# Performance work log

Hardware: AMD Instinct MI355X
Metric: run time of the kernel (lower is better)

Reference implementation:

```python
import jax, jax.numpy as jnp
import numpy as np

H = 4          # num_heads
DK = 128       # head_k_dim = hidden*expand_k/H = 1024*0.5/4
DV = 256       # head_v_dim = hidden*expand_v/H
LOW_RANK = 16  # gate_low_rank_dim
GATE_NORM = 16.0  # gate_logit_normalizer
CHUNK = 64
EPS = 1e-5


def setup_inputs() -> dict:
    key = jax.random.key(0)
    ks = jax.random.split(key, 10)
    Dm = 1024
    Kd, Vd = H * DK, H * DV  # key_dim=512, value_dim=1024
    def lin(k, fan_in, fan_out):
        return jax.random.normal(k, (fan_in, fan_out), jnp.float32) * (fan_in ** -0.5)
    return {
        "x": jax.random.normal(ks[0], (4, 2048, Dm), jnp.float32),
        "Wq": lin(ks[1], Dm, Kd),
        "Wk": lin(ks[2], Dm, Kd),
        "Wv": lin(ks[3], Dm, Vd),
        "Wg": lin(ks[4], Dm, Vd),            # output gate proj
        "Wgk1": lin(ks[5], Dm, LOW_RANK),     # low-rank gate proj (no bias)
        "Wgk2": lin(ks[6], LOW_RANK, Kd),     # second gate proj (with bias)
        "bgk2": jnp.zeros((Kd,), jnp.float32),
        "Wo": lin(ks[7], Vd, Dm),
        "gnw": jnp.ones((DV,), jnp.float32),  # FusedRMSNormGated weight
    }


def _gla_chunk(q, k, v, gk):
    """Exact chunkwise evaluation of the GLA recurrence:
       S_t = diag(exp(gk_t)) S_{t-1} + k_t^T v_t;  o_t = scale * q_t S_t.
       q,k,gk: [B,T,H,DK], v: [B,T,H,DV]."""
    B, T, _, _ = q.shape
    NC, C = T // CHUNK, CHUNK
    scale = DK ** -0.5
    def chunks(a):  # [B,T,H,D] -> [NC,B,H,C,D]
        return a.reshape(B, NC, C, H, a.shape[-1]).transpose(1, 0, 3, 2, 4)
    qc, kc, vc, gc = chunks(q), chunks(k), chunks(v), chunks(gk)
    G = jnp.cumsum(gc, axis=-2)                    # within-chunk cumulative log-decay
    qg = qc * jnp.exp(G) * scale                   # q_i exp(G_i)
    k_intra = kc * jnp.exp(-G)                     # k_j exp(-G_j)
    kg = kc * jnp.exp(G[..., -1:, :] - G)          # k_j exp(G_C - G_j) for state update
    g_last = jnp.exp(G[..., -1, :])                # exp(G_C): per-chunk total decay
    # intra-chunk causal attention (diagonal included)
    A = jnp.einsum('nbhik,nbhjk->nbhij', qg, k_intra)
    A = jnp.where(jnp.tril(jnp.ones((C, C), bool)), A, 0.0)
    o_intra = jnp.einsum('nbhij,nbhjv->nbhiv', A, vc)
    def step(S, inp):
        qg_, kg_, v_, gl_, oi_ = inp
        o = oi_ + jnp.einsum('bhck,bhkv->bhcv', qg_, S)
        S = S * gl_[..., :, None] + jnp.einsum('bhck,bhcv->bhkv', kg_, v_)
        return S, o
    S0 = jnp.zeros((B, H, DK, DV), q.dtype)
    _, o = jax.lax.scan(step, S0, (qg, kg, vc, g_last, o_intra))
    return o.transpose(1, 0, 3, 2, 4).reshape(B, T, H, DV)


def reference(x, Wq, Wk, Wv, Wg, Wgk1, Wgk2, bgk2, Wo, gnw):
    B, T, Dm = x.shape
    q = (x @ Wq).reshape(B, T, H, DK)
    k = (x @ Wk).reshape(B, T, H, DK)
    v = (x @ Wv).reshape(B, T, H, DV)
    gk = jax.nn.log_sigmoid((x @ Wgk1) @ Wgk2 + bgk2) / GATE_NORM
    gk = gk.reshape(B, T, H, DK)
    o = _gla_chunk(q, k, v, gk)                              # [B,T,H,DV]
    g = (x @ Wg).reshape(B, T, H, DV)
    # FusedRMSNormGated: RMSNorm(o) * weight * swish(g)
    o = o * jax.lax.rsqrt(jnp.mean(o * o, axis=-1, keepdims=True) + EPS) * gnw
    o = o * (g * jax.nn.sigmoid(g))
    return o.reshape(B, T, H * DV) @ Wo
```

## Files before the change

kernel.cpp:

```cpp
#include <hip/hip_runtime.h>
#include <hip/hip_bf16.h>
#include <stdint.h>

#define B_  4
#define T_  2048
#define DM  1024
#define H_  4
#define DK_ 128
#define DV_ 256
#define KD  512
#define VD  1024
#define NCH 32
#define CC  64
#define BT  8192
#define SCALE 0.08838834764831845f
#define GNORM_INV 0.0625f

typedef __attribute__((ext_vector_type(8))) short short8;
typedef __attribute__((ext_vector_type(4))) float f32x4;
typedef uint32_t u32;
typedef unsigned short ushort_t;

__device__ inline ushort_t f2b(float f) {
    u32 u = __builtin_bit_cast(u32, f);
    u32 r = (u + 0x7fffu + ((u >> 16) & 1u)) >> 16;
    return (ushort_t)r;
}
__device__ inline void unpack2(u32 u, float& lo, float& hi) {
    lo = __builtin_bit_cast(float, u << 16);
    hi = __builtin_bit_cast(float, u & 0xffff0000u);
}

__global__ __launch_bounds__(256)
void cvtx(const float* __restrict__ x, ushort_t* __restrict__ xb, int n) {
    int idx = (blockIdx.x * 256 + threadIdx.x) * 8;
    if (idx >= n) return;
    float4 a = *(const float4*)&x[idx];
    float4 b = *(const float4*)&x[idx + 4];
    uint4 p;
    p.x = (u32)f2b(a.x) | ((u32)f2b(a.y) << 16);
    p.y = (u32)f2b(a.z) | ((u32)f2b(a.w) << 16);
    p.z = (u32)f2b(b.x) | ((u32)f2b(b.y) << 16);
    p.w = (u32)f2b(b.z) | ((u32)f2b(b.w) << 16);
    *(uint4*)&xb[idx] = p;
}

__global__ __launch_bounds__(256)
void tcvt(const float* __restrict__ W, ushort_t* __restrict__ Wt, int K, int N) {
    __shared__ float tile[32][33];
    const int k0 = blockIdx.x * 32, n0 = blockIdx.y * 32;
    const int r = threadIdx.x >> 3, c4 = (threadIdx.x & 7) * 4;
    float4 wv = *(const float4*)&W[(size_t)(k0 + r) * N + n0 + c4];
    tile[r][c4 + 0] = wv.x; tile[r][c4 + 1] = wv.y;
    tile[r][c4 + 2] = wv.z; tile[r][c4 + 3] = wv.w;
    __syncthreads();
    u32 lo = (u32)f2b(tile[c4 + 0][r]) | ((u32)f2b(tile[c4 + 1][r]) << 16);
    u32 hi = (u32)f2b(tile[c4 + 2][r]) | ((u32)f2b(tile[c4 + 3][r]) << 16);
    uint2 o2; o2.x = lo; o2.y = hi;
    *(uint2*)&Wt[(size_t)(n0 + r) * K + k0 + c4] = o2;
}

template<int OUTBF>
__global__ __launch_bounds__(256)
void gemm_bf16(const ushort_t* __restrict__ A, const ushort_t* __restrict__ Bt,
               void* __restrict__ Cout, int M, int N, int K) {
    __shared__ ushort_t Al[128 * 40];
    __shared__ ushort_t Bl[128 * 40];
    const int t = threadIdx.x;
    const int wave = t >> 6, lane = t & 63;
    const int wr = wave >> 1, wc = wave & 1;
    const int row0 = blockIdx.x * 128, col0 = blockIdx.y * 128;
    const int lr = t >> 2;
    const int lk8 = (t & 3) * 8;
    const int lm = lane & 15, lk = (lane >> 4) * 8;

    f32x4 acc[4][4];
    #pragma unroll
    for (int i = 0; i < 4; ++i)
        #pragma unroll
        for (int j = 0; j < 4; ++j) acc[i][j] = f32x4{0.f, 0.f, 0.f, 0.f};

    const ushort_t* Ap = A + (size_t)row0 * K;
    const ushort_t* Bp = Bt + (size_t)col0 * K;

    for (int k0 = 0; k0 < K; k0 += 32) {
        __syncthreads();
        #pragma unroll
        for (int m = 0; m < 2; ++m) {
            int r = m * 64 + lr;
            uint4 av = *(const uint4*)(Ap + (size_t)r * K + k0 + lk8);
            *(uint4*)(&Al[r * 40 + lk8]) = av;
            uint4 bv = *(const uint4*)(Bp + (size_t)r * K + k0 + lk8);
            *(uint4*)(&Bl[r * 40 + lk8]) = bv;
        }
        __syncthreads();
        short8 af[4], bfr[4];
        #pragma unroll
        for (int f = 0; f < 4; ++f)
            af[f] = *(const short8*)(&Al[(wr * 64 + f * 16 + lm) * 40 + lk]);
        #pragma unroll
        for (int f = 0; f < 4; ++f)
            bfr[f] = *(const short8*)(&Bl[(wc * 64 + f * 16 + lm) * 40 + lk]);
        #pragma unroll
        for (int i = 0; i < 4; ++i)
            #pragma unroll
            for (int j = 0; j < 4; ++j)
                acc[i][j] = __builtin_amdgcn_mfma_f32_16x16x32_bf16(af[i], bfr[j], acc[i][j], 0, 0, 0);
    }
    const int orow = row0 + wr * 64 + (lane >> 4) * 4;
    const int ocol = col0 + wc * 64 + lm;
    #pragma unroll
    for (int i = 0; i < 4; ++i)
        #pragma unroll
        for (int j = 0; j < 4; ++j)
            #pragma unroll
            for (int e = 0; e < 4; ++e) {
                int rr = orow + i * 16 + e, cc = ocol + j * 16;
                if (OUTBF) ((ushort_t*)Cout)[(size_t)rr * N + cc] = f2b(acc[i][j][e]);
                else       ((float*)Cout)[(size_t)rr * N + cc]   = acc[i][j][e];
            }
}

__global__ __launch_bounds__(256)
void lowrank_kernel(const float* __restrict__ x, const float* __restrict__ W1,
                    float* __restrict__ tmp) {
    const int t = threadIdx.x;
    const int r = t >> 4, c = t & 15;
    const int row = blockIdx.x * 16 + r;
    const float* xp = x + (size_t)row * DM;
    float acc = 0.f;
    for (int kk = 0; kk < DM; kk += 4) {
        float4 xv = *(const float4*)(xp + kk);
        acc += xv.x * W1[(kk + 0) * 16 + c];
        acc += xv.y * W1[(kk + 1) * 16 + c];
        acc += xv.z * W1[(kk + 2) * 16 + c];
        acc += xv.w * W1[(kk + 3) * 16 + c];
    }
    tmp[row * 16 + c] = acc;
}

__global__ __launch_bounds__(256)
void gatek_kernel(const float* __restrict__ tmp, const float* __restrict__ W2,
                  const float* __restrict__ bias, float* __restrict__ gk) {
    const int idx = blockIdx.x * 256 + threadIdx.x;
    const int bt = idx >> 9, c = idx & 511;
    float z = bias[c];
    #pragma unroll
    for (int j = 0; j < 16; ++j)
        z += tmp[bt * 16 + j] * W2[j * KD + c];
    float ls = fminf(z, 0.f) - log1pf(expf(-fabsf(z)));
    gk[idx] = ls * GNORM_INV;
}

__global__ __launch_bounds__(128)
void gateprep_kernel(const float* __restrict__ q, const float* __restrict__ kf,
                     const float* __restrict__ gk,
                     ushort_t* __restrict__ qgb, ushort_t* __restrict__ kib,
                     ushort_t* __restrict__ kgb, float* __restrict__ glast) {
    const int bid = blockIdx.x;
    const int c = bid & 31, bh = bid >> 5;
    const int b = bh >> 2, h = bh & 3;
    const int d = threadIdx.x;
    const int t0 = b * T_ + c * CC;
    const int gbase = t0 * KD + h * DK_ + d;
    const int obase = bid * (CC * DK_) + d;

    float total = 0.f;
    for (int i = 0; i < CC; ++i) total += gk[gbase + i * KD];

    float G = 0.f;
    for (int i = 0; i < CC; ++i) {
        const int gi = gbase + i * KD;
        G += gk[gi];
        float qv = q[gi], kv = kf[gi];
        qgb[obase + i * DK_] = f2b(qv * expf(G) * SCALE);
        kib[obase + i * DK_] = f2b(kv * expf(-G));
        kgb[obase + i * DK_] = f2b(kv * expf(total - G));
    }
    glast[bid * DK_ + d] = expf(total);
}

__global__ __launch_bounds__(256)
void vtrans_kernel(const ushort_t* __restrict__ vbf, ushort_t* __restrict__ vT) {
    __shared__ ushort_t vl[64][264];
    const int bid = blockIdx.x;
    const int c = bid & 31, bh = bid >> 5;
    const int b = bh >> 2, h = bh & 3;
    const int t0 = b * T_ + c * CC;
    const int t = threadIdx.x;

    #pragma unroll
    for (int m = 0; m < 8; ++m) {
        int p = t + m * 256;
        int j = p >> 5, d8 = (p & 31) * 8;
        *(uint4*)&vl[j][d8] = *(const uint4*)&vbf[(size_t)(t0 + j) * VD + h * DV_ + d8];
    }
    __syncthreads();

    const size_t outb = (size_t)bid * (256 * 64);
    #pragma unroll
    for (int it = 0; it < 2; ++it) {
        int dv = it * 128 + (t >> 1);
        int j0 = (t & 1) * 32;
        u32 vv[16];
        #pragma unroll
        for (int wi = 0; wi < 16; ++wi)
            vv[wi] = (u32)vl[j0 + 2 * wi][dv] | ((u32)vl[j0 + 2 * wi + 1][dv] << 16);
        ushort_t* dst = &vT[outb + (size_t)dv * 64 + j0];
        *(uint4*)(dst + 0)  = make_uint4(vv[0], vv[1], vv[2], vv[3]);
        *(uint4*)(dst + 8)  = make_uint4(vv[4], vv[5], vv[6], vv[7]);
        *(uint4*)(dst + 16) = make_uint4(vv[8], vv[9], vv[10], vv[11]);
        *(uint4*)(dst + 24) = make_uint4(vv[12], vv[13], vv[14], vv[15]);
    }
}

__global__ __launch_bounds__(256)
void chunk_state(const ushort_t* __restrict__ kgb, const ushort_t* __restrict__ vT,
                 ushort_t* __restrict__ Sst) {
    __shared__ ushort_t kgT[128 * 72];
    const int bid = blockIdx.x;
    const int t = threadIdx.x;
    const size_t kgbase = (size_t)bid * (CC * DK_);
    const size_t vtbase = (size_t)bid * (256 * 64);
    const size_t sbase  = (size_t)bid * (256 * 128);

    #pragma unroll
    for (int m = 0; m < 4; ++m) {
        int p = t + m * 256;
        int j = p >> 4, d0 = (p & 15) * 8;
        uint4 r = *(const uint4*)&kgb[kgbase + (size_t)j * DK_ + d0];
        kgT[(d0 + 0) * 72 + j] = (ushort_t)(r.x & 0xffff);
        kgT[(d0 + 1) * 72 + j] = (ushort_t)(r.x >> 16);
        kgT[(d0 + 2) * 72 + j] = (ushort_t)(r.y & 0xffff);
        kgT[(d0 + 3) * 72 + j] = (ushort_t)(r.y >> 16);
        kgT[(d0 + 4) * 72 + j] = (ushort_t)(r.z & 0xffff);
        kgT[(d0 + 5) * 72 + j] = (ushort_t)(r.z >> 16);
        kgT[(d0 + 6) * 72 + j] = (ushort_t)(r.w & 0xffff);
        kgT[(d0 + 7) * 72 + j] = (ushort_t)(r.w >> 16);
    }
    __syncthreads();

    const int w = t >> 6, lane = t & 63;
    const int lm = lane & 15, lg = lane >> 4;
    #pragma unroll
    for (int mm = 0; mm < 4; ++mm) {
        const int mt = w * 4 + mm;
        short8 a0 = *(const short8*)&vT[vtbase + (size_t)(mt * 16 + lm) * 64 + lg * 8];
        short8 a1 = *(const short8*)&vT[vtbase + (size_t)(mt * 16 + lm) * 64 + 32 + lg * 8];
        #pragma unroll
        for (int n = 0; n < 8; ++n) {
            f32x4 acc = {0.f, 0.f, 0.f, 0.f};
            short8 b0 = *(const short8*)&kgT[(n * 16 + lm) * 72 + lg * 8];
            short8 b1 = *(const short8*)&kgT[(n * 16 + lm) * 72 + 32 + lg * 8];
            acc = __builtin_amdgcn_mfma_f32_16x16x32_bf16(a0, b0, acc, 0, 0, 0);
            acc = __builtin_amdgcn_mfma_f32_16x16x32_bf16(a1, b1, acc, 0, 0, 0);
            #pragma unroll
            for (int e = 0; e < 4; ++e)
                Sst[sbase + (size_t)(mt * 16 + lg * 4 + e) * 128 + n * 16 + lm] = f2b(acc[e]);
        }
    }
}

__global__ __launch_bounds__(256)
void scan_combine(ushort_t* __restrict__ Sst, const float* __restrict__ glast) {
    const int bid = blockIdx.x;
    const int dvt = bid & 7, bh = bid >> 3;
    const int t = threadIdx.x;
    const int dv = dvt * 32 + (t >> 3);
    const int dk0 = (t & 7) * 16;

    float P[16];
    #pragma unroll
    for (int e = 0; e < 16; ++e) P[e] = 0.f;

    for (int c = 0; c < NCH; ++c) {
        const size_t base = ((size_t)(bh * NCH + c) * 256 + dv) * 128 + dk0;
        uint4 m0 = *(const uint4*)&Sst[base];
        uint4 m1 = *(const uint4*)&Sst[base + 8];
        u32 wd[8];
        #pragma unroll
        for (int e = 0; e < 8; ++e)
            wd[e] = (u32)f2b(P[2 * e]) | ((u32)f2b(P[2 * e + 1]) << 16);
        *(uint4*)&Sst[base]     = make_uint4(wd[0], wd[1], wd[2], wd[3]);
        *(uint4*)&Sst[base + 8] = make_uint4(wd[4], wd[5], wd[6], wd[7]);
        float mv[16];
        unpack2(m0.x, mv[0], mv[1]);   unpack2(m0.y, mv[2], mv[3]);
        unpack2(m0.z, mv[4], mv[5]);   unpack2(m0.w, mv[6], mv[7]);
        unpack2(m1.x, mv[8], mv[9]);   unpack2(m1.y, mv[10], mv[11]);
        unpack2(m1.z, mv[12], mv[13]); unpack2(m1.w, mv[14], mv[15]);
        const float* glp = &glast[(size_t)(bh * NCH + c) * DK_ + dk0];
        float4 g0 = *(const float4*)&glp[0];
        float4 g1 = *(const float4*)&glp[4];
        float4 g2 = *(const float4*)&glp[8];
        float4 g3 = *(const float4*)&glp[12];
        float gl[16] = {g0.x, g0.y, g0.z, g0.w, g1.x, g1.y, g1.z, g1.w,
                        g2.x, g2.y, g2.z, g2.w, g3.x, g3.y, g3.z, g3.w};
        #pragma unroll
        for (int e = 0; e < 16; ++e) P[e] = gl[e] * P[e] + mv[e];
    }
}

__global__ __launch_bounds__(256)
void fused_chunk(const ushort_t* __restrict__ qgb, const ushort_t* __restrict__ kib,
                 const ushort_t* __restrict__ vT, const ushort_t* __restrict__ Sst,
                 float* __restrict__ o) {
    __shared__ __align__(16) ushort_t lds[24064];
    ushort_t* stg = lds;
    ushort_t* vq  = lds + 10752;
    ushort_t* Al  = lds + 17408;

    const int bid = blockIdx.x;
    const int c = bid & 31, bh = bid >> 5;
    const int b = bh >> 2, h = bh & 3;
    const int t0 = b * T_ + c * CC;
    const int t = threadIdx.x;
    const int w = t >> 6, lane = t & 63;
    const int lm = lane & 15, lg = lane >> 4;
    const int m0 = w * 16;

    const size_t qbase  = (size_t)bid * (CC * DK_);
    const size_t vtbase = (size_t)bid * (256 * 64);
    const size_t sbase  = (size_t)bid * (256 * 128);

    short8 qf[4];
    #pragma unroll
    for (int kk = 0; kk < 4; ++kk)
        qf[kk] = *(const short8*)&qgb[qbase + (size_t)(m0 + lm) * DK_ + kk * 32 + lg * 8];

    #pragma unroll
    for (int m = 0; m < 4; ++m) {
        int p = t + m * 256;
        int j = p >> 4, d0 = (p & 15) * 8;
        *(uint4*)&stg[j * 168 + d0] = *(const uint4*)&kib[qbase + (size_t)j * DK_ + d0];
    }
    __syncthreads();

    f32x4 accA[4];
    #pragma unroll
    for (int jt = 0; jt < 4; ++jt) accA[jt] = f32x4{0.f, 0.f, 0.f, 0.f};
    #pragma unroll
    for (int jt = 0; jt < 4; ++jt)
        #pragma unroll
        for (int kk = 0; kk < 4; ++kk) {
            short8 bfrag = *(const short8*)&stg[(jt * 16 + lm) * 168 + kk * 32 + lg * 8];
            accA[jt] = __builtin_amdgcn_mfma_f32_16x16x32_bf16(qf[kk], bfrag, accA[jt], 0, 0, 0);
        }
    #pragma unroll
    for (int jt = 0; jt < 4; ++jt)
        #pragma unroll
        for (int e = 0; e < 4; ++e) {
            int i = m0 + lg * 4 + e, j = jt * 16 + lm;
            Al[i * 104 + j] = f2b(j <= i ? accA[jt][e] : 0.f);
        }
    __syncthreads();

    short8 af[2];
    #pragma unroll
    for (int kk = 0; kk < 2; ++kk)
        af[kk] = *(const short8*)&Al[(m0 + lm) * 104 + kk * 32 + lg * 8];

    #pragma unroll 1
    for (int qq = 0; qq < 4; ++qq) {
        #pragma unroll
        for (int m = 0; m < 2; ++m) {
            int p = t + m * 256;
            int dvr = p >> 3, d0 = (p & 7) * 8;
            *(uint4*)&vq[dvr * 104 + d0] =
                *(const uint4*)&vT[vtbase + (size_t)(qq * 64 + dvr) * 64 + d0];
        }
        #pragma unroll
        for (int m = 0; m < 4; ++m) {
            int p = t + m * 256;
            int dvr = p >> 4, d0 = (p & 15) * 8;
            *(uint4*)&stg[dvr * 168 + d0] =
                *(const uint4*)&Sst[sbase + (size_t)(qq * 64 + dvr) * 128 + d0];
        }
        __syncthreads();
        #pragma unroll
        for (int n = 0; n < 4; ++n) {
            f32x4 acc = {0.f, 0.f, 0.f, 0.f};
            #pragma unroll
            for (int kk = 0; kk < 2; ++kk) {
                short8 bfrag = *(const short8*)&vq[(n * 16 + lm) * 104 + kk * 32 + lg * 8];
                acc = __builtin_amdgcn_mfma_f32_16x16x32_bf16(af[kk], bfrag, acc, 0, 0, 0);
            }
            #pragma unroll
            for (int kk = 0; kk < 4; ++kk) {
                short8 bfrag = *(const short8*)&stg[(n * 16 + lm) * 168 + kk * 32 + lg * 8];
                acc = __builtin_amdgcn_mfma_f32_16x16x32_bf16(qf[kk], bfrag, acc, 0, 0, 0);
            }
            #pragma unroll
            for (int e = 0; e < 4; ++e)
                o[(size_t)(t0 + m0 + lg * 4 + e) * VD + h * DV_ + qq * 64 + n * 16 + lm] = acc[e];
        }
        __syncthreads();
    }
}

__global__ __launch_bounds__(256)
void normgate_kernel(const float* __restrict__ o, const ushort_t* __restrict__ gbf,
                     const float* __restrict__ gnw, ushort_t* __restrict__ obf) {
    const int t = threadIdx.x;
    const int w = t >> 6, lane = t & 63;
    const int row = blockIdx.x * 4 + w;
    const size_t base = (size_t)row * DV_ + lane * 4;

    float4 ov = *(const float4*)&o[base];
    float ssq = ov.x * ov.x + ov.y * ov.y + ov.z * ov.z + ov.w * ov.w;
    #pragma unroll
    for (int off = 32; off > 0; off >>= 1) ssq += __shfl_xor(ssq, off);
    const float rms = rsqrtf(ssq * (1.0f / DV_) + 1e-5f);

    uint2 gv2 = *(const uint2*)&gbf[base];
    float g0, g1, g2, g3;
    unpack2(gv2.x, g0, g1); unpack2(gv2.y, g2, g3);
    float4 wv = *(const float4*)&gnw[lane * 4];
    float o0 = ov.x * rms * wv.x * (g0 / (1.f + expf(-g0)));
    float o1 = ov.y * rms * wv.y * (g1 / (1.f + expf(-g1)));
    float o2 = ov.z * rms * wv.z * (g2 / (1.f + expf(-g2)));
    float o3 = ov.w * rms * wv.w * (g3 / (1.f + expf(-g3)));
    uint2 p;
    p.x = (u32)f2b(o0) | ((u32)f2b(o1) << 16);
    p.y = (u32)f2b(o2) | ((u32)f2b(o3) << 16);
    *(uint2*)&obf[base] = p;
}

extern "C" void kernel_launch(void* const* d_in, const int* in_sizes, int n_in,
                              void* d_out, int out_size, void* d_ws, size_t ws_size,
                              hipStream_t stream) {
    const float* x    = (const float*)d_in[0];
    const float* Wq   = (const float*)d_in[1];
    const float* Wk   = (const float*)d_in[2];
    const float* Wv   = (const float*)d_in[3];
    const float* Wg   = (const float*)d_in[4];
    const float* Wgk1 = (const float*)d_in[5];
    const float* Wgk2 = (const float*)d_in[6];
    const float* bgk2 = (const float*)d_in[7];
    const float* Wo   = (const float*)d_in[8];
    const float* gnw  = (const float*)d_in[9];

    float* ws = (float*)d_ws;
    float* q      = ws;
    float* kf     = ws + 4194304;
    float* gk     = ws + 8388608;
    ushort_t* vT  = (ushort_t*)(ws + 12582912);
    ushort_t* Sst = (ushort_t*)(ws + 16777216);
    ushort_t* vbf = (ushort_t*)(ws + 16777216);
    ushort_t* wbf = (ushort_t*)(ws + 20971520);
    ushort_t* gbf = (ushort_t*)(ws + 8388608);
    ushort_t* obf = (ushort_t*)(ws + 16777216);
    float* o      = ws;
    ushort_t* xbf = (ushort_t*)(ws + 25165824);
    ushort_t* qgb = (ushort_t*)(ws + 29360128);
    ushort_t* kib = (ushort_t*)(ws + 31457280);
    ushort_t* kgb = (ushort_t*)(ws + 33554432);
    float* tmp16  = ws + 35651584;
    float* glast  = ws + 35782656;

    cvtx<<<4096, 256, 0, stream>>>(x, xbf, BT * DM);

    tcvt<<<dim3(32, 16), 256, 0, stream>>>(Wq, wbf, DM, KD);
    gemm_bf16<0><<<dim3(64, 4), 256, 0, stream>>>(xbf, wbf, q, BT, KD, DM);
    tcvt<<<dim3(32, 16), 256, 0, stream>>>(Wk, wbf, DM, KD);
    gemm_bf16<0><<<dim3(64, 4), 256, 0, stream>>>(xbf, wbf, kf, BT, KD, DM);
    tcvt<<<dim3(32, 32), 256, 0, stream>>>(Wv, wbf, DM, VD);
    gemm_bf16<1><<<dim3(64, 8), 256, 0, stream>>>(xbf, wbf, vbf, BT, VD, DM);

    lowrank_kernel<<<512, 256, 0, stream>>>(x, Wgk1, tmp16);
    gatek_kernel<<<16384, 256, 0, stream>>>(tmp16, Wgk2, bgk2, gk);
    gateprep_kernel<<<512, 128, 0, stream>>>(q, kf, gk, qgb, kib, kgb, glast);

    vtrans_kernel<<<512, 256, 0, stream>>>(vbf, vT);

    tcvt<<<dim3(32, 32), 256, 0, stream>>>(Wg, wbf, DM, VD);
    gemm_bf16<1><<<dim3(64, 8), 256, 0, stream>>>(xbf, wbf, gbf, BT, VD, DM);

    chunk_state<<<512, 256, 0, stream>>>(kgb, vT, Sst);
    scan_combine<<<128, 256, 0, stream>>>(Sst, glast);
    fused_chunk<<<512, 256, 0, stream>>>(qgb, kib, vT, Sst, o);

    normgate_kernel<<<8192, 256, 0, stream>>>(o, gbf, gnw, obf);
    tcvt<<<dim3(32, 32), 256, 0, stream>>>(Wo, wbf, VD, DM);
    gemm_bf16<0><<<dim3(64, 8), 256, 0, stream>>>(obf, wbf, (float*)d_out, BT, DM, VD);
}
```

Before: 412.1 us.

## Use direct global-to-LDS loads in GEMM, split lowrank, widen scan, store o in bf16

The GEMM now loads its A and B tiles straight into LDS with global_load_lds, which removes the register staging, and drops the row padding from 40 to 32. The lowrank projection gives each row its own block, splits K across 16 thread groups and reduces through shared memory, so it exposes far more parallelism. scan_combine uses twice as many blocks with half the work per thread, and fused_chunk writes o as bf16 so normgate reads half the bytes. Without padding the GEMM fragment reads may hit LDS bank conflicts, and storing o in bf16 adds rounding before the RMSNorm.

```diff
diff --git a/kernel.cpp b/kernel.cpp
--- a/kernel.cpp
+++ b/kernel.cpp
@@ -30,6 +30,11 @@
     lo = __builtin_bit_cast(float, u << 16);
     hi = __builtin_bit_cast(float, u & 0xffff0000u);
 }
+__device__ inline void gload_lds16(const void* g, void* l) {
+    __builtin_amdgcn_global_load_lds(
+        (const __attribute__((address_space(1))) uint32_t*)g,
+        (__attribute__((address_space(3))) uint32_t*)l, 16, 0, 0);
+}
 
 __global__ __launch_bounds__(256)
 void cvtx(const float* __restrict__ x, ushort_t* __restrict__ xb, int n) {
@@ -64,15 +69,21 @@
 __global__ __launch_bounds__(256)
 void gemm_bf16(const ushort_t* __restrict__ A, const ushort_t* __restrict__ Bt,
                void* __restrict__ Cout, int M, int N, int K) {
-    __shared__ ushort_t Al[128 * 40];
-    __shared__ ushort_t Bl[128 * 40];
+    __shared__ ushort_t Al[128 * 32];
+    __shared__ ushort_t Bl[128 * 32];
     const int t = threadIdx.x;
     const int wave = t >> 6, lane = t & 63;
     const int wr = wave >> 1, wc = wave & 1;
     const int row0 = blockIdx.x * 128, col0 = blockIdx.y * 128;
-    const int lr = t >> 2;
-    const int lk8 = (t & 3) * 8;
     const int lm = lane & 15, lk = (lane >> 4) * 8;
+
+    const int b0 = t * 16;
+    const int r0 = b0 >> 6, c0 = (b0 & 63) >> 1;
+    const int r1 = (4096 + b0) >> 6, c1 = ((4096 + b0) & 63) >> 1;
+    ushort_t* ldsA0 = &Al[(wave * 1024) >> 1];
+    ushort_t* ldsA1 = &Al[(4096 + wave * 1024) >> 1];
+    ushort_t* ldsB0 = &Bl[(wave * 1024) >> 1];
+    ushort_t* ldsB1 = &Bl[(4096 + wave * 1024) >> 1];
 
     f32x4 acc[4][4];
     #pragma unroll
@@ -85,22 +96,18 @@
 
     for (int k0 = 0; k0 < K; k0 += 32) {
         __syncthreads();
-        #pragma unroll
-        for (int m = 0; m < 2; ++m) {
-            int r = m * 64 + lr;
-            uint4 av = *(const uint4*)(Ap + (size_t)r * K + k0 + lk8);
-            *(uint4*)(&Al[r * 40 + lk8]) = av;
-            uint4 bv = *(const uint4*)(Bp + (size_t)r * K + k0 + lk8);
-            *(uint4*)(&Bl[r * 40 + lk8]) = bv;
-        }
+        gload_lds16(Ap + (size_t)r0 * K + k0 + c0, ldsA0);
+        gload_lds16(Ap + (size_t)r1 * K + k0 + c1, ldsA1);
+        gload_lds16(Bp + (size_t)r0 * K + k0 + c0, ldsB0);
+        gload_lds16(Bp + (size_t)r1 * K + k0 + c1, ldsB1);
         __syncthreads();
         short8 af[4], bfr[4];
         #pragma unroll
         for (int f = 0; f < 4; ++f)
-            af[f] = *(const short8*)(&Al[(wr * 64 + f * 16 + lm) * 40 + lk]);
+            af[f] = *(const short8*)(&Al[(wr * 64 + f * 16 + lm) * 32 + lk]);
         #pragma unroll
         for (int f = 0; f < 4; ++f)
-            bfr[f] = *(const short8*)(&Bl[(wc * 64 + f * 16 + lm) * 40 + lk]);
+            bfr[f] = *(const short8*)(&Bl[(wc * 64 + f * 16 + lm) * 32 + lk]);
         #pragma unroll
         for (int i = 0; i < 4; ++i)
             #pragma unroll
@@ -124,19 +131,27 @@
 __global__ __launch_bounds__(256)
 void lowrank_kernel(const float* __restrict__ x, const float* __restrict__ W1,
                     float* __restrict__ tmp) {
-    const int t = threadIdx.x;
-    const int r = t >> 4, c = t & 15;
-    const int row = blockIdx.x * 16 + r;
-    const float* xp = x + (size_t)row * DM;
+    __shared__ float part[16][20];
+    const int row = blockIdx.x;
+    const int t = threadIdx.x;
+    const int ks = t >> 4, c = t & 15;
+    const float* xp = x + (size_t)row * DM + ks * 64;
+    const float* wp0 = W1 + (size_t)(ks * 64) * 16 + c;
     float acc = 0.f;
-    for (int kk = 0; kk < DM; kk += 4) {
-        float4 xv = *(const float4*)(xp + kk);
-        acc += xv.x * W1[(kk + 0) * 16 + c];
-        acc += xv.y * W1[(kk + 1) * 16 + c];
-        acc += xv.z * W1[(kk + 2) * 16 + c];
-        acc += xv.w * W1[(kk + 3) * 16 + c];
-    }
-    tmp[row * 16 + c] = acc;
+    #pragma unroll
+    for (int i = 0; i < 16; ++i) {
+        float4 xv = *(const float4*)&xp[i * 4];
+        const float* wp = wp0 + i * 64;
+        acc += xv.x * wp[0] + xv.y * wp[16] + xv.z * wp[32] + xv.w * wp[48];
+    }
+    part[ks][c] = acc;
+    __syncthreads();
+    if (t < 16) {
+        float s = 0.f;
+        #pragma unroll
+        for (int i = 0; i < 16; ++i) s += part[i][t];
+        tmp[row * 16 + t] = s;
+    }
 }
 
 __global__ __launch_bounds__(256)
@@ -264,46 +279,39 @@
 __global__ __launch_bounds__(256)
 void scan_combine(ushort_t* __restrict__ Sst, const float* __restrict__ glast) {
     const int bid = blockIdx.x;
-    const int dvt = bid & 7, bh = bid >> 3;
-    const int t = threadIdx.x;
-    const int dv = dvt * 32 + (t >> 3);
-    const int dk0 = (t & 7) * 16;
-
-    float P[16];
-    #pragma unroll
-    for (int e = 0; e < 16; ++e) P[e] = 0.f;
+    const int dvt = bid & 15, bh = bid >> 4;
+    const int t = threadIdx.x;
+    const int dv = dvt * 16 + (t >> 4);
+    const int dk0 = (t & 15) * 8;
+
+    float P[8];
+    #pragma unroll
+    for (int e = 0; e < 8; ++e) P[e] = 0.f;
 
     for (int c = 0; c < NCH; ++c) {
         const size_t base = ((size_t)(bh * NCH + c) * 256 + dv) * 128 + dk0;
         uint4 m0 = *(const uint4*)&Sst[base];
-        uint4 m1 = *(const uint4*)&Sst[base + 8];
-        u32 wd[8];
-        #pragma unroll
-        for (int e = 0; e < 8; ++e)
+        u32 wd[4];
+        #pragma unroll
+        for (int e = 0; e < 4; ++e)
             wd[e] = (u32)f2b(P[2 * e]) | ((u32)f2b(P[2 * e + 1]) << 16);
-        *(uint4*)&Sst[base]     = make_uint4(wd[0], wd[1], wd[2], wd[3]);
-        *(uint4*)&Sst[base + 8] = make_uint4(wd[4], wd[5], wd[6], wd[7]);
-        float mv[16];
-        unpack2(m0.x, mv[0], mv[1]);   unpack2(m0.y, mv[2], mv[3]);
-        unpack2(m0.z, mv[4], mv[5]);   unpack2(m0.w, mv[6], mv[7]);
-        unpack2(m1.x, mv[8], mv[9]);   unpack2(m1.y, mv[10], mv[11]);
-        unpack2(m1.z, mv[12], mv[13]); unpack2(m1.w, mv[14], mv[15]);
+        *(uint4*)&Sst[base] = make_uint4(wd[0], wd[1], wd[2], wd[3]);
+        float mv[8];
+        unpack2(m0.x, mv[0], mv[1]); unpack2(m0.y, mv[2], mv[3]);
+        unpack2(m0.z, mv[4], mv[5]); unpack2(m0.w, mv[6], mv[7]);
         const float* glp = &glast[(size_t)(bh * NCH + c) * DK_ + dk0];
         float4 g0 = *(const float4*)&glp[0];
         float4 g1 = *(const float4*)&glp[4];
-        float4 g2 = *(const float4*)&glp[8];
-        float4 g3 = *(const float4*)&glp[12];
-        float gl[16] = {g0.x, g0.y, g0.z, g0.w, g1.x, g1.y, g1.z, g1.w,
-                        g2.x, g2.y, g2.z, g2.w, g3.x, g3.y, g3.z, g3.w};
-        #pragma unroll
-        for (int e = 0; e < 16; ++e) P[e] = gl[e] * P[e] + mv[e];
+        float gl[8] = {g0.x, g0.y, g0.z, g0.w, g1.x, g1.y, g1.z, g1.w};
+        #pragma unroll
+        for (int e = 0; e < 8; ++e) P[e] = gl[e] * P[e] + mv[e];
     }
 }
 
 __global__ __launch_bounds__(256)
 void fused_chunk(const ushort_t* __restrict__ qgb, const ushort_t* __restrict__ kib,
                  const ushort_t* __restrict__ vT, const ushort_t* __restrict__ Sst,
-                 float* __restrict__ o) {
+                 ushort_t* __restrict__ ob) {
     __shared__ __align__(16) ushort_t lds[24064];
     ushort_t* stg = lds;
     ushort_t* vq  = lds + 10752;
@@ -391,22 +399,24 @@
             }
             #pragma unroll
             for (int e = 0; e < 4; ++e)
-                o[(size_t)(t0 + m0 + lg * 4 + e) * VD + h * DV_ + qq * 64 + n * 16 + lm] = acc[e];
+                ob[(size_t)(t0 + m0 + lg * 4 + e) * VD + h * DV_ + qq * 64 + n * 16 + lm] = f2b(acc[e]);
         }
         __syncthreads();
     }
 }
 
 __global__ __launch_bounds__(256)
-void normgate_kernel(const float* __restrict__ o, const ushort_t* __restrict__ gbf,
+void normgate_kernel(const ushort_t* __restrict__ ob, const ushort_t* __restrict__ gbf,
                      const float* __restrict__ gnw, ushort_t* __restrict__ obf) {
     const int t = threadIdx.x;
     const int w = t >> 6, lane = t & 63;
     const int row = blockIdx.x * 4 + w;
     const size_t base = (size_t)row * DV_ + lane * 4;
 
-    float4 ov = *(const float4*)&o[base];
-    float ssq = ov.x * ov.x + ov.y * ov.y + ov.z * ov.z + ov.w * ov.w;
+    uint2 ov2 = *(const uint2*)&ob[base];
+    float o0v, o1v, o2v, o3v;
+    unpack2(ov2.x, o0v, o1v); unpack2(ov2.y, o2v, o3v);
+    float ssq = o0v * o0v + o1v * o1v + o2v * o2v + o3v * o3v;
     #pragma unroll
     for (int off = 32; off > 0; off >>= 1) ssq += __shfl_xor(ssq, off);
     const float rms = rsqrtf(ssq * (1.0f / DV_) + 1e-5f);
@@ -415,13 +425,13 @@
     float g0, g1, g2, g3;
     unpack2(gv2.x, g0, g1); unpack2(gv2.y, g2, g3);
     float4 wv = *(const float4*)&gnw[lane * 4];
-    float o0 = ov.x * rms * wv.x * (g0 / (1.f + expf(-g0)));
-    float o1 = ov.y * rms * wv.y * (g1 / (1.f + expf(-g1)));
-    float o2 = ov.z * rms * wv.z * (g2 / (1.f + expf(-g2)));
-    float o3 = ov.w * rms * wv.w * (g3 / (1.f + expf(-g3)));
+    float r0 = o0v * rms * wv.x * (g0 / (1.f + expf(-g0)));
+    float r1 = o1v * rms * wv.y * (g1 / (1.f + expf(-g1)));
+    float r2 = o2v * rms * wv.z * (g2 / (1.f + expf(-g2)));
+    float r3 = o3v * rms * wv.w * (g3 / (1.f + expf(-g3)));
     uint2 p;
-    p.x = (u32)f2b(o0) | ((u32)f2b(o1) << 16);
-    p.y = (u32)f2b(o2) | ((u32)f2b(o3) << 16);
+    p.x = (u32)f2b(r0) | ((u32)f2b(r1) << 16);
+    p.y = (u32)f2b(r2) | ((u32)f2b(r3) << 16);
     *(uint2*)&obf[base] = p;
 }
 
@@ -449,7 +459,7 @@
     ushort_t* wbf = (ushort_t*)(ws + 20971520);
     ushort_t* gbf = (ushort_t*)(ws + 8388608);
     ushort_t* obf = (ushort_t*)(ws + 16777216);
-    float* o      = ws;
+    ushort_t* ob  = (ushort_t*)ws;
     ushort_t* xbf = (ushort_t*)(ws + 25165824);
     ushort_t* qgb = (ushort_t*)(ws + 29360128);
     ushort_t* kib = (ushort_t*)(ws + 31457280);
@@ -466,7 +476,7 @@
     tcvt<<<dim3(32, 32), 256, 0, stream>>>(Wv, wbf, DM, VD);
     gemm_bf16<1><<<dim3(64, 8), 256, 0, stream>>>(xbf, wbf, vbf, BT, VD, DM);
 
-    lowrank_kernel<<<512, 256, 0, stream>>>(x, Wgk1, tmp16);
+    lowrank_kernel<<<8192, 256, 0, stream>>>(x, Wgk1, tmp16);
     gatek_kernel<<<16384, 256, 0, stream>>>(tmp16, Wgk2, bgk2, gk);
     gateprep_kernel<<<512, 128, 0, stream>>>(q, kf, gk, qgb, kib, kgb, glast);
 
@@ -476,10 +486,10 @@
     gemm_bf16<1><<<dim3(64, 8), 256, 0, stream>>>(xbf, wbf, gbf, BT, VD, DM);
 
     chunk_state<<<512, 256, 0, stream>>>(kgb, vT, Sst);
-    scan_combine<<<128, 256, 0, stream>>>(Sst, glast);
-    fused_chunk<<<512, 256, 0, stream>>>(qgb, kib, vT, Sst, o);
-
-    normgate_kernel<<<8192, 256, 0, stream>>>(o, gbf, gnw, obf);
+    scan_combine<<<256, 256, 0, stream>>>(Sst, glast);
+    fused_chunk<<<512, 256, 0, stream>>>(qgb, kib, vT, Sst, ob);
+
+    normgate_kernel<<<8192, 256, 0, stream>>>(ob, gbf, gnw, obf);
     tcvt<<<dim3(32, 32), 256, 0, stream>>>(Wo, wbf, VD, DM);
     gemm_bf16<0><<<dim3(64, 8), 256, 0, stream>>>(obf, wbf, (float*)d_out, BT, DM, VD);
 }
```

After: 402.6 us. 1.02x faster.
